# Kernel optimization log

Hardware: AMD Instinct MI355X
Metric: run time of the kernel (lower is better)

The kernel has to match this reference:

```python
import jax, jax.numpy as jnp
import numpy as np
import math

S, B, D, H = 2048, 2, 1024, 16
DK = D // H


def setup_inputs() -> dict:
    key = jax.random.key(0)
    ks = jax.random.split(key, 13)
    scale = 1.0 / math.sqrt(D)
    inp = {
        "query": jax.random.normal(ks[0], (S, B, D), jnp.float32),
        "key": jax.random.normal(ks[1], (S, B, D), jnp.float32),
        "value": jax.random.normal(ks[2], (S, B, D), jnp.float32),
        "mask": jax.random.normal(ks[3], (B, S, S), jnp.float32),
        # four Linear(d_model, d_model) layers: q, k, v, out. torch convention W:(out,in)
        "Wq": jax.random.normal(ks[4], (D, D), jnp.float32) * scale,
        "bq": jax.random.normal(ks[5], (D,), jnp.float32) * scale,
        "Wk": jax.random.normal(ks[6], (D, D), jnp.float32) * scale,
        "bk": jax.random.normal(ks[7], (D,), jnp.float32) * scale,
        "Wv": jax.random.normal(ks[8], (D, D), jnp.float32) * scale,
        "bv": jax.random.normal(ks[9], (D,), jnp.float32) * scale,
        "Wo": jax.random.normal(ks[10], (D, D), jnp.float32) * scale,
        "bo": jax.random.normal(ks[11], (D,), jnp.float32) * scale,
    }
    return inp


def reference(query, key, value, mask, Wq, bq, Wk, bk, Wv, bv, Wo, bo):
    # inputs are (tokens S, batch B, d_model D)
    def proj(x, W, b):  # torch Linear: x @ W.T + b, then split heads -> (B,H,S,DK)
        y = jnp.einsum('sbd,ed->sbe', x, W) + b
        return y.reshape(S, B, H, DK).transpose(1, 2, 0, 3)

    q = proj(query, Wq, bq)
    k = proj(key, Wk, bk)
    v = proj(value, Wv, bv)

    scores = jnp.einsum('bhsd,bhtd->bhst', q, k) / math.sqrt(DK)
    scores = scores + mask[:, None, :, :]  # broadcast over heads
    p_attn = jax.nn.softmax(scores, axis=-1)  # (B,H,S,S)

    x = jnp.einsum('bhst,bhtd->bhsd', p_attn, v)  # (B,H,S,DK)
    x = x.transpose(2, 0, 1, 3).reshape(S, B, D)  # (S,B,D)
    out = jnp.einsum('sbd,ed->sbe', x, Wo) + bo

    attn = p_attn.mean(axis=1)  # mean over heads -> (B,S,S)
    return out, attn
```

## Files before the change

kernel.cpp:

```cpp
#include <hip/hip_runtime.h>
#include <hip/hip_bf16.h>


#define S_LEN 2048
#define BATCH 2
#define DMODEL 1024
#define NH 16
#define DKH 64
#define SCALE 0.125f
#define QSCALE 0.180336878f
#define FMAX 20.0f
#define KSTRIDE 72

typedef __bf16 bf16_t;
typedef __attribute__((ext_vector_type(8))) __bf16 bf16x8;
typedef __attribute__((ext_vector_type(8))) unsigned short u16x8;
typedef __attribute__((ext_vector_type(4))) float f32x4;

__device__ __forceinline__ unsigned short f32_bf16_rne(float f) {
  union { float f; unsigned int u; } v; v.f = f;
  unsigned int u = v.u;
  u += 0x7fffu + ((u >> 16) & 1u);
  return (unsigned short)(u >> 16);
}
__device__ __forceinline__ float bf16u_f32(unsigned short us) {
  union { unsigned int u; float f; } v; v.u = ((unsigned int)us) << 16;
  return v.f;
}
__device__ __forceinline__ f32x4 mfma_bf16(bf16x8 a, bf16x8 b, f32x4 c) {
  return __builtin_amdgcn_mfma_f32_16x16x32_bf16(a, b, c, 0, 0, 0);
}
__device__ __forceinline__ float exp2_fast(float x) {
#if __has_builtin(__builtin_amdgcn_exp2f)
  return __builtin_amdgcn_exp2f(x);
#else
  return __expf(x * 0.69314718f);
#endif
}
__device__ __forceinline__ void gload16(const bf16_t* g, unsigned short* l) {
  __builtin_amdgcn_global_load_lds(
      (const __attribute__((address_space(1))) void*)g,
      (__attribute__((address_space(3))) void*)l, 16, 0, 0);
}

__global__ __launch_bounds__(256) void cvt_w_kernel(
    const float* __restrict__ w0, const float* __restrict__ w1,
    const float* __restrict__ w2, const float* __restrict__ w3,
    bf16_t* __restrict__ o0, bf16_t* __restrict__ o1,
    bf16_t* __restrict__ o2, bf16_t* __restrict__ o3) {
  const float* src; bf16_t* dst;
  switch (blockIdx.y) {
    case 0: src = w0; dst = o0; break;
    case 1: src = w1; dst = o1; break;
    case 2: src = w2; dst = o2; break;
    default: src = w3; dst = o3; break;
  }
  int i = (blockIdx.x * 256 + threadIdx.x) * 4;
  float4 v = *(const float4*)(src + i);
  union { unsigned short u[4]; uint2 q; } r;
  r.u[0] = f32_bf16_rne(v.x); r.u[1] = f32_bf16_rne(v.y);
  r.u[2] = f32_bf16_rne(v.z); r.u[3] = f32_bf16_rne(v.w);
  *(uint2*)(dst + i) = r.q;
}

__global__ __launch_bounds__(256) void cvt_x_kernel(
    const float* __restrict__ x0, const float* __restrict__ x1,
    const float* __restrict__ x2,
    bf16_t* __restrict__ o0, bf16_t* __restrict__ o1, bf16_t* __restrict__ o2) {
  const float* src; bf16_t* dst;
  switch (blockIdx.y) {
    case 0: src = x0; dst = o0; break;
    case 1: src = x1; dst = o1; break;
    default: src = x2; dst = o2; break;
  }
  int i = (blockIdx.x * 256 + threadIdx.x) * 4;
  float4 v = *(const float4*)(src + i);
  union { unsigned short u[4]; uint2 q; } r;
  r.u[0] = f32_bf16_rne(v.x); r.u[1] = f32_bf16_rne(v.y);
  r.u[2] = f32_bf16_rne(v.z); r.u[3] = f32_bf16_rne(v.w);
  *(uint2*)(dst + i) = r.q;
}

__global__ __launch_bounds__(256) void cvt_mask_kernel(
    const float* __restrict__ m, bf16_t* __restrict__ o) {
  int i = (blockIdx.x * 256 + threadIdx.x) * 4;
  float4 v = *(const float4*)(m + i);
  union { unsigned short u[4]; uint2 q; } r;
  r.u[0] = f32_bf16_rne(__expf(v.x - FMAX));
  r.u[1] = f32_bf16_rne(__expf(v.y - FMAX));
  r.u[2] = f32_bf16_rne(__expf(v.z - FMAX));
  r.u[3] = f32_bf16_rne(__expf(v.w - FMAX));
  *(uint2*)(o + i) = r.q;
}

__global__ __launch_bounds__(256) void proj_kernel(
    const bf16_t* __restrict__ Xq, const bf16_t* __restrict__ Xk, const bf16_t* __restrict__ Xv,
    const bf16_t* __restrict__ Wqb, const bf16_t* __restrict__ Wkb, const bf16_t* __restrict__ Wvb,
    const float* __restrict__ bq, const float* __restrict__ bk, const float* __restrict__ bv,
    bf16_t* __restrict__ qo, bf16_t* __restrict__ ko, bf16_t* __restrict__ vTo) {
  int mode = blockIdx.z;
  const bf16_t* X = (mode == 0) ? Xq : (mode == 1) ? Xk : Xv;
  const bf16_t* W = (mode == 0) ? Wqb : (mode == 1) ? Wkb : Wvb;
  const float* bias = (mode == 0) ? bq : (mode == 1) ? bk : bv;

  __shared__ __align__(16) unsigned short Alds[128 * 32];
  __shared__ __align__(16) unsigned short Blds[128 * 32];

  int tid = threadIdx.x;
  int wv = tid >> 6, lane = tid & 63, quad = lane >> 4, col = lane & 15;
  int wr = wv >> 1, wc = wv & 1;
  int rowbase = blockIdx.x * 128;
  int colbase = blockIdx.y * 128;

  int srow = tid >> 2;
  int sk8 = (tid & 3) * 8;
  const bf16_t* ga0 = X + (size_t)(rowbase + srow) * DMODEL + sk8;
  const bf16_t* gb0 = W + (size_t)(colbase + srow) * DMODEL + sk8;
  unsigned short* la0 = Alds + tid * 8;
  unsigned short* lb0 = Blds + tid * 8;

  f32x4 acc[4][4] = {};

  for (int k0 = 0; k0 < DMODEL; k0 += 32) {
    gload16(ga0 + k0, la0);
    gload16(ga0 + 64 * DMODEL + k0, la0 + 2048);
    gload16(gb0 + k0, lb0);
    gload16(gb0 + 64 * DMODEL + k0, lb0 + 2048);
    __syncthreads();

    union { u16x8 u; bf16x8 v; } af[4], bfr[4];
#pragma unroll
    for (int mi = 0; mi < 4; ++mi)
      af[mi].u = *(const u16x8*)(Alds + (wr * 64 + mi * 16 + col) * 32 + quad * 8);
#pragma unroll
    for (int ni = 0; ni < 4; ++ni)
      bfr[ni].u = *(const u16x8*)(Blds + (wc * 64 + ni * 16 + col) * 32 + quad * 8);
#pragma unroll
    for (int mi = 0; mi < 4; ++mi)
#pragma unroll
      for (int ni = 0; ni < 4; ++ni)
        acc[mi][ni] = mfma_bf16(af[mi].v, bfr[ni].v, acc[mi][ni]);
    __syncthreads();
  }

  float biasv[4];
#pragma unroll
  for (int ni = 0; ni < 4; ++ni)
    biasv[ni] = bias[colbase + wc * 64 + ni * 16 + col];

#pragma unroll
  for (int mi = 0; mi < 4; ++mi)
#pragma unroll
    for (int ni = 0; ni < 4; ++ni)
#pragma unroll
      for (int r = 0; r < 4; ++r) {
        int grow = rowbase + wr * 64 + mi * 16 + quad * 4 + r;
        int gcol = colbase + wc * 64 + ni * 16 + col;
        float val = acc[mi][ni][r] + biasv[ni];
        if (mode == 0) val *= QSCALE;
        unsigned short us = f32_bf16_rne(val);
        int s = grow >> 1, bb = grow & 1;
        int h = gcol >> 6, dk = gcol & 63;
        if (mode == 2) {
          ((unsigned short*)vTo)[((size_t)(bb * NH + h) * DKH + dk) * S_LEN + s] = us;
        } else {
          unsigned short* dst = (unsigned short*)(mode == 0 ? qo : ko);
          dst[((size_t)(bb * NH + h) * S_LEN + s) * DKH + dk] = us;
        }
      }
}

__global__ __launch_bounds__(512) void flash_kernel(
    const bf16_t* __restrict__ emb,
    const bf16_t* __restrict__ q_ws, const bf16_t* __restrict__ k_ws,
    const bf16_t* __restrict__ vT_ws,
    bf16_t* __restrict__ x_ws, float* __restrict__ rl_ws) {
  int tid = threadIdx.x;
  int w = tid >> 6, lane = tid & 63, quad = lane >> 4, col = lane & 15;
  int b = blockIdx.y, h = blockIdx.z;
  int s0 = blockIdx.x * 128 + w * 16;
  int bh = b * NH + h;

  __shared__ __align__(16) unsigned short Klds[64 * KSTRIDE];
  __shared__ __align__(16) unsigned short Vlds[64 * KSTRIDE];
  __shared__ __align__(16) unsigned short Plds[8][16 * KSTRIDE];
  unsigned short* pw = &Plds[w][0];

  const bf16_t* qh = q_ws + (size_t)bh * S_LEN * DKH;
  const bf16_t* kh = k_ws + (size_t)bh * S_LEN * DKH;
  const bf16_t* vh = vT_ws + (size_t)bh * DKH * S_LEN;
  const unsigned short* emrow = (const unsigned short*)emb +
      (size_t)b * S_LEN * S_LEN + (size_t)(s0 + quad * 4) * S_LEN;

  bf16x8 qf0 = *(const bf16x8*)(qh + (s0 + col) * DKH + quad * 8);
  bf16x8 qf1 = *(const bf16x8*)(qh + (s0 + col) * DKH + 32 + quad * 8);

  int srow = w * 8 + (lane >> 3), schunk = lane & 7;
  const unsigned short* kg = (const unsigned short*)(kh + (size_t)srow * DKH + schunk * 8);
  const unsigned short* vg = (const unsigned short*)(vh + (size_t)srow * S_LEN + schunk * 8);
  u16x8* kl = (u16x8*)(Klds + srow * KSTRIDE + schunk * 8);
  u16x8* vl = (u16x8*)(Vlds + srow * KSTRIDE + schunk * 8);

  int psw = (quad & 2) ? 16 : 0;
  int rsw = (col & 8) ? 16 : 0;

  f32x4 xacc[4] = {};
  f32x4 lacc = {};

  u16x8 kpre = *(const u16x8*)kg;
  u16x8 vpre = *(const u16x8*)vg;

  for (int t0 = 0; t0 < S_LEN; t0 += 64) {
    *kl = kpre;
    *vl = vpre;
    __syncthreads();

    if (t0 + 64 < S_LEN) {
      kpre = *(const u16x8*)(kg + (size_t)(t0 + 64) * DKH);
      vpre = *(const u16x8*)(vg + (t0 + 64));
    }

    float emv[4][4];
#pragma unroll
    for (int j = 0; j < 4; ++j)
#pragma unroll
      for (int r = 0; r < 4; ++r)
        emv[j][r] = bf16u_f32(emrow[r * S_LEN + t0 + j * 16 + col]);

    f32x4 C[4];
#pragma unroll
    for (int j = 0; j < 4; ++j) {
      int row = j * 16 + col;
      union { u16x8 u; bf16x8 v; } kb0, kb1;
      kb0.u = *(const u16x8*)(Klds + row * KSTRIDE + quad * 8);
      kb1.u = *(const u16x8*)(Klds + row * KSTRIDE + 32 + quad * 8);
      f32x4 z = {};
      C[j] = mfma_bf16(qf1, kb1.v, mfma_bf16(qf0, kb0.v, z));
    }

#pragma unroll
    for (int j = 0; j < 4; ++j) {
      float p0 = exp2_fast(C[j][0]) * emv[j][0];
      float p1 = exp2_fast(C[j][1]) * emv[j][1];
      float p2 = exp2_fast(C[j][2]) * emv[j][2];
      float p3 = exp2_fast(C[j][3]) * emv[j][3];
      lacc[0] += p0; lacc[1] += p1; lacc[2] += p2; lacc[3] += p3;
      unsigned int w01, w23;
      asm("v_cvt_pk_bf16_f32 %0, %1, %2" : "=v"(w01) : "v"(p0), "v"(p1));
      asm("v_cvt_pk_bf16_f32 %0, %1, %2" : "=v"(w23) : "v"(p2), "v"(p3));
      int tsw = (j * 16 + col) ^ psw;
      int rb = quad * 4;
      pw[(rb + 0) * KSTRIDE + tsw] = (unsigned short)(w01 & 0xffffu);
      pw[(rb + 1) * KSTRIDE + tsw] = (unsigned short)(w01 >> 16);
      pw[(rb + 2) * KSTRIDE + tsw] = (unsigned short)(w23 & 0xffffu);
      pw[(rb + 3) * KSTRIDE + tsw] = (unsigned short)(w23 >> 16);
    }

    union { u16x8 u; bf16x8 v; } pa0, pa1;
    pa0.u = *(const u16x8*)(pw + col * KSTRIDE + ((quad * 8) ^ rsw));
    pa1.u = *(const u16x8*)(pw + col * KSTRIDE + (32 + ((quad * 8) ^ rsw)));

#pragma unroll
    for (int ni = 0; ni < 4; ++ni) {
      int row = ni * 16 + col;
      union { u16x8 u; bf16x8 v; } vb0, vb1;
      vb0.u = *(const u16x8*)(Vlds + row * KSTRIDE + quad * 8);
      vb1.u = *(const u16x8*)(Vlds + row * KSTRIDE + 32 + quad * 8);
      xacc[ni] = mfma_bf16(pa1.v, vb1.v, mfma_bf16(pa0.v, vb0.v, xacc[ni]));
    }
    __syncthreads();
  }

  for (int d = 1; d < 16; d <<= 1)
    for (int r = 0; r < 4; ++r) lacc[r] += __shfl_xor(lacc[r], d, 64);
  float rl[4];
  for (int r = 0; r < 4; ++r) rl[r] = 1.0f / lacc[r];

  unsigned short* xo = (unsigned short*)x_ws;
  for (int ni = 0; ni < 4; ++ni)
    for (int r = 0; r < 4; ++r) {
      int sr = s0 + quad * 4 + r;
      xo[((size_t)bh * S_LEN + sr) * DKH + ni * 16 + col] =
          f32_bf16_rne(xacc[ni][r] * rl[r]);
    }
  if (col == 0)
    for (int r = 0; r < 4; ++r)
      rl_ws[bh * S_LEN + s0 + quad * 4 + r] = rl[r];
}

__global__ __launch_bounds__(256) void attn_kernel(
    const bf16_t* __restrict__ emb,
    const bf16_t* __restrict__ q_ws, const bf16_t* __restrict__ k_ws,
    const float* __restrict__ rl_ws,
    float* __restrict__ attn_out) {
  int tid = threadIdx.x;
  int w = tid >> 6, lane = tid & 63, quad = lane >> 4, col = lane & 15;
  int b = blockIdx.y;
  int s0 = blockIdx.x * 64 + w * 16;
  int t_base = blockIdx.z * 128;

  __shared__ __align__(16) unsigned short Klds[128 * KSTRIDE];

  const unsigned short* emrow = (const unsigned short*)emb +
      (size_t)b * S_LEN * S_LEN + (size_t)(s0 + quad * 4) * S_LEN + t_base;
  float emf[8][4];
  for (int j = 0; j < 8; ++j)
    for (int r = 0; r < 4; ++r)
      emf[j][r] = bf16u_f32(emrow[r * S_LEN + j * 16 + col]);

  f32x4 acc[8] = {};

  int srow_a = w * 8 + (lane >> 3), schunk_a = (lane & 7) * 8;
  const bf16_t* kh0 = k_ws + (size_t)(b * NH) * S_LEN * DKH;

  u16x8 kpre[4];
#pragma unroll
  for (int i = 0; i < 4; ++i)
    kpre[i] = *(const u16x8*)(kh0 + (size_t)(t_base + i * 32 + srow_a) * DKH + schunk_a);

  for (int h = 0; h < NH; ++h) {
    int bh = b * NH + h;
    const bf16_t* qh = q_ws + (size_t)bh * S_LEN * DKH;

#pragma unroll
    for (int i = 0; i < 4; ++i)
      *(u16x8*)(Klds + (i * 32 + srow_a) * KSTRIDE + schunk_a) = kpre[i];
    __syncthreads();

    if (h + 1 < NH) {
      const bf16_t* khn = kh0 + (size_t)(h + 1) * S_LEN * DKH;
#pragma unroll
      for (int i = 0; i < 4; ++i)
        kpre[i] = *(const u16x8*)(khn + (size_t)(t_base + i * 32 + srow_a) * DKH + schunk_a);
    }

    bf16x8 qf0 = *(const bf16x8*)(qh + (s0 + col) * DKH + quad * 8);
    bf16x8 qf1 = *(const bf16x8*)(qh + (s0 + col) * DKH + 32 + quad * 8);
    float rl4[4];
    for (int r = 0; r < 4; ++r) rl4[r] = rl_ws[bh * S_LEN + s0 + quad * 4 + r];

#pragma unroll
    for (int j = 0; j < 8; ++j) {
      int row = j * 16 + col;
      union { u16x8 u; bf16x8 v; } kb0, kb1;
      kb0.u = *(const u16x8*)(Klds + row * KSTRIDE + quad * 8);
      kb1.u = *(const u16x8*)(Klds + row * KSTRIDE + 32 + quad * 8);
      f32x4 z = {};
      f32x4 C = mfma_bf16(qf1, kb1.v, mfma_bf16(qf0, kb0.v, z));
#pragma unroll
      for (int r = 0; r < 4; ++r) {
        float t = exp2_fast(C[r]) * emf[j][r];
        acc[j][r] = fmaf(t, rl4[r], acc[j][r]);
      }
    }
    __syncthreads();
  }

  for (int j = 0; j < 8; ++j)
    for (int r = 0; r < 4; ++r)
      attn_out[((size_t)b * S_LEN + s0 + quad * 4 + r) * S_LEN + t_base + j * 16 + col] =
          acc[j][r] * (1.0f / NH);
}

__global__ __launch_bounds__(256) void outproj_kernel(
    const bf16_t* __restrict__ x_ws, const bf16_t* __restrict__ Wob,
    const float* __restrict__ bo, float* __restrict__ out) {
  __shared__ __align__(16) unsigned short Alds[128 * 32];
  __shared__ __align__(16) unsigned short Blds[128 * 32];

  int tid = threadIdx.x;
  int wv = tid >> 6, lane = tid & 63, quad = lane >> 4, col = lane & 15;
  int wr = wv >> 1, wc = wv & 1;
  int rowbase = blockIdx.x * 128;
  int colbase = blockIdx.y * 128;

  int srow = tid >> 2;
  int sk8 = (tid & 3) * 8;
  int r0 = rowbase + srow;
  int s0a = r0 >> 1, b0a = r0 & 1;
  int r1 = r0 + 64;
  int s1a = r1 >> 1, b1a = r1 & 1;
  const bf16_t* gb0 = Wob + (size_t)(colbase + srow) * DMODEL + sk8;
  unsigned short* la0 = Alds + tid * 8;
  unsigned short* lb0 = Blds + tid * 8;

  f32x4 acc[4][4] = {};

  for (int k0 = 0; k0 < DMODEL; k0 += 32) {
    int h = k0 >> 6, dk = (k0 & 63) + sk8;
    gload16(x_ws + ((size_t)(b0a * NH + h) * S_LEN + s0a) * DKH + dk, la0);
    gload16(x_ws + ((size_t)(b1a * NH + h) * S_LEN + s1a) * DKH + dk, la0 + 2048);
    gload16(gb0 + k0, lb0);
    gload16(gb0 + 64 * DMODEL + k0, lb0 + 2048);
    __syncthreads();

    union { u16x8 u; bf16x8 v; } af[4], bfr[4];
#pragma unroll
    for (int mi = 0; mi < 4; ++mi)
      af[mi].u = *(const u16x8*)(Alds + (wr * 64 + mi * 16 + col) * 32 + quad * 8);
#pragma unroll
    for (int ni = 0; ni < 4; ++ni)
      bfr[ni].u = *(const u16x8*)(Blds + (wc * 64 + ni * 16 + col) * 32 + quad * 8);
#pragma unroll
    for (int mi = 0; mi < 4; ++mi)
#pragma unroll
      for (int ni = 0; ni < 4; ++ni)
        acc[mi][ni] = mfma_bf16(af[mi].v, bfr[ni].v, acc[mi][ni]);
    __syncthreads();
  }

  float biasv[4];
#pragma unroll
  for (int ni = 0; ni < 4; ++ni)
    biasv[ni] = bo[colbase + wc * 64 + ni * 16 + col];

#pragma unroll
  for (int mi = 0; mi < 4; ++mi)
#pragma unroll
    for (int ni = 0; ni < 4; ++ni)
#pragma unroll
      for (int r = 0; r < 4; ++r) {
        int grow = rowbase + wr * 64 + mi * 16 + quad * 4 + r;
        int gcol = colbase + wc * 64 + ni * 16 + col;
        out[(size_t)grow * DMODEL + gcol] = acc[mi][ni][r] + biasv[ni];
      }
}

extern "C" void kernel_launch(void* const* d_in, const int* in_sizes, int n_in,
                              void* d_out, int out_size, void* d_ws, size_t ws_size,
                              hipStream_t stream) {
  const float* query = (const float*)d_in[0];
  const float* key_  = (const float*)d_in[1];
  const float* value = (const float*)d_in[2];
  const float* mask  = (const float*)d_in[3];
  const float* Wq = (const float*)d_in[4];
  const float* bq = (const float*)d_in[5];
  const float* Wk = (const float*)d_in[6];
  const float* bk = (const float*)d_in[7];
  const float* Wv = (const float*)d_in[8];
  const float* bv = (const float*)d_in[9];
  const float* Wo = (const float*)d_in[10];
  const float* bo = (const float*)d_in[11];

  char* ws = (char*)d_ws;
  bf16_t* q_ws  = (bf16_t*)(ws + 0);
  bf16_t* k_ws  = (bf16_t*)(ws + 8388608);
  bf16_t* vT_ws = (bf16_t*)(ws + 16777216);
  bf16_t* x_ws  = (bf16_t*)(ws + 25165824);
  float*  rl_ws = (float*)(ws + 33554432);
  bf16_t* Wqb = (bf16_t*)(ws + 33816576);
  bf16_t* Wkb = (bf16_t*)(ws + 35913728);
  bf16_t* Wvb = (bf16_t*)(ws + 38010880);
  bf16_t* Wob = (bf16_t*)(ws + 40108032);
  bf16_t* Xq_b = x_ws;
  bf16_t* Xk_b = (bf16_t*)(ws + 42205184);
  bf16_t* Xv_b = (bf16_t*)(ws + 50593792);
  bf16_t* emb  = (bf16_t*)(ws + 42205184);

  float* outp  = (float*)d_out;
  float* attnp = outp + (size_t)S_LEN * BATCH * DMODEL;

  cvt_w_kernel<<<dim3(1024, 4), 256, 0, stream>>>(Wq, Wk, Wv, Wo, Wqb, Wkb, Wvb, Wob);
  cvt_x_kernel<<<dim3(4096, 3), 256, 0, stream>>>(query, key_, value, Xq_b, Xk_b, Xv_b);
  proj_kernel<<<dim3(32, 8, 3), 256, 0, stream>>>(Xq_b, Xk_b, Xv_b,
                                                  Wqb, Wkb, Wvb, bq, bk, bv,
                                                  q_ws, k_ws, vT_ws);
  cvt_mask_kernel<<<dim3(8192), 256, 0, stream>>>(mask, emb);
  flash_kernel<<<dim3(16, 2, 16), 512, 0, stream>>>(emb, q_ws, k_ws, vT_ws, x_ws, rl_ws);
  attn_kernel<<<dim3(32, 2, 16), 256, 0, stream>>>(emb, q_ws, k_ws, rl_ws, attnp);
  outproj_kernel<<<dim3(32, 8), 256, 0, stream>>>(x_ws, Wob, bo, outp);
}
```

Measured before the change: 350.3 us.

## Restructure flash kernel: transposed MFMA keeps P in registers, two query tiles per wave

The flash kernel now computes S^T = K·Q^T, so each lane holds probabilities along the key dimension. K rows are loaded into LDS in a permuted order so those probabilities can feed the P·V MFMA straight from registers, which removes the per-wave LDS round trip for P. Each wave now handles two 16-row query tiles, so every K/V fragment read from LDS is reused twice. Blocks shrink to 256 threads on a 1D grid whose index mapping spreads (batch, head) pairs across neighbouring blocks. The cost is more registers per wave and fewer waves per block.

```diff
diff --git a/kernel.cpp b/kernel.cpp
--- a/kernel.cpp
+++ b/kernel.cpp
@@ -15,6 +15,7 @@
 typedef __bf16 bf16_t;
 typedef __attribute__((ext_vector_type(8))) __bf16 bf16x8;
 typedef __attribute__((ext_vector_type(8))) unsigned short u16x8;
+typedef __attribute__((ext_vector_type(4))) unsigned short u16x4;
 typedef __attribute__((ext_vector_type(4))) float f32x4;
 
 __device__ __forceinline__ unsigned short f32_bf16_rne(float f) {
@@ -36,6 +37,11 @@
 #else
   return __expf(x * 0.69314718f);
 #endif
+}
+__device__ __forceinline__ unsigned int cvtpk(float lo, float hi) {
+  unsigned int r;
+  asm("v_cvt_pk_bf16_f32 %0, %1, %2" : "=v"(r) : "v"(lo), "v"(hi));
+  return r;
 }
 __device__ __forceinline__ void gload16(const bf16_t* g, unsigned short* l) {
   __builtin_amdgcn_global_load_lds(
@@ -170,122 +176,145 @@
       }
 }
 
-__global__ __launch_bounds__(512) void flash_kernel(
+__global__ __launch_bounds__(256) void flash_kernel(
     const bf16_t* __restrict__ emb,
     const bf16_t* __restrict__ q_ws, const bf16_t* __restrict__ k_ws,
     const bf16_t* __restrict__ vT_ws,
     bf16_t* __restrict__ x_ws, float* __restrict__ rl_ws) {
   int tid = threadIdx.x;
   int w = tid >> 6, lane = tid & 63, quad = lane >> 4, col = lane & 15;
-  int b = blockIdx.y, h = blockIdx.z;
-  int s0 = blockIdx.x * 128 + w * 16;
-  int bh = b * NH + h;
+
+  int bid = blockIdx.x;
+  int wi = bid >> 3;
+  int bh = (bid & 7) * 4 + (wi & 3);
+  int qblk = wi >> 2;
+  int b = bh >> 4;
+  int s0 = qblk * 128 + w * 32;
+  int sA = s0, sB = s0 + 16;
 
   __shared__ __align__(16) unsigned short Klds[64 * KSTRIDE];
   __shared__ __align__(16) unsigned short Vlds[64 * KSTRIDE];
-  __shared__ __align__(16) unsigned short Plds[8][16 * KSTRIDE];
-  unsigned short* pw = &Plds[w][0];
 
   const bf16_t* qh = q_ws + (size_t)bh * S_LEN * DKH;
   const bf16_t* kh = k_ws + (size_t)bh * S_LEN * DKH;
   const bf16_t* vh = vT_ws + (size_t)bh * DKH * S_LEN;
-  const unsigned short* emrow = (const unsigned short*)emb +
-      (size_t)b * S_LEN * S_LEN + (size_t)(s0 + quad * 4) * S_LEN;
-
-  bf16x8 qf0 = *(const bf16x8*)(qh + (s0 + col) * DKH + quad * 8);
-  bf16x8 qf1 = *(const bf16x8*)(qh + (s0 + col) * DKH + 32 + quad * 8);
-
-  int srow = w * 8 + (lane >> 3), schunk = lane & 7;
-  const unsigned short* kg = (const unsigned short*)(kh + (size_t)srow * DKH + schunk * 8);
-  const unsigned short* vg = (const unsigned short*)(vh + (size_t)srow * S_LEN + schunk * 8);
-  u16x8* kl = (u16x8*)(Klds + srow * KSTRIDE + schunk * 8);
-  u16x8* vl = (u16x8*)(Vlds + srow * KSTRIDE + schunk * 8);
-
-  int psw = (quad & 2) ? 16 : 0;
-  int rsw = (col & 8) ? 16 : 0;
-
-  f32x4 xacc[4] = {};
-  f32x4 lacc = {};
-
-  u16x8 kpre = *(const u16x8*)kg;
-  u16x8 vpre = *(const u16x8*)vg;
+  const unsigned short* emA = (const unsigned short*)emb +
+      (size_t)b * S_LEN * S_LEN + (size_t)(sA + col) * S_LEN;
+  const unsigned short* emB = emA + (size_t)16 * S_LEN;
+
+  bf16x8 qA0 = *(const bf16x8*)(qh + (sA + col) * DKH + quad * 8);
+  bf16x8 qA1 = *(const bf16x8*)(qh + (sA + col) * DKH + 32 + quad * 8);
+  bf16x8 qB0 = *(const bf16x8*)(qh + (sB + col) * DKH + quad * 8);
+  bf16x8 qB1 = *(const bf16x8*)(qh + (sB + col) * DKH + 32 + quad * 8);
+
+  int row1 = tid >> 3, row2 = row1 + 32;
+  int ch = (tid & 7) * 8;
+  int pi1 = (row1 & 32) + ((row1 & 16) >> 2) + ((row1 & 12) << 1) + (row1 & 3);
+  int pi2 = (row2 & 32) + ((row2 & 16) >> 2) + ((row2 & 12) << 1) + (row2 & 3);
+  const unsigned short* kg1 = (const unsigned short*)kh + (size_t)pi1 * DKH + ch;
+  const unsigned short* kg2 = (const unsigned short*)kh + (size_t)pi2 * DKH + ch;
+  const unsigned short* vg1 = (const unsigned short*)vh + (size_t)row1 * S_LEN + ch;
+  const unsigned short* vg2 = (const unsigned short*)vh + (size_t)row2 * S_LEN + ch;
+  u16x8* kl1 = (u16x8*)(Klds + row1 * KSTRIDE + ch);
+  u16x8* kl2 = (u16x8*)(Klds + row2 * KSTRIDE + ch);
+  u16x8* vl1 = (u16x8*)(Vlds + row1 * KSTRIDE + ch);
+  u16x8* vl2 = (u16x8*)(Vlds + row2 * KSTRIDE + ch);
+
+  f32x4 xA[4] = {}, xB[4] = {};
+  float lsumA = 0.0f, lsumB = 0.0f;
+
+  u16x8 kp1 = *(const u16x8*)kg1;
+  u16x8 kp2 = *(const u16x8*)kg2;
+  u16x8 vp1 = *(const u16x8*)vg1;
+  u16x8 vp2 = *(const u16x8*)vg2;
 
   for (int t0 = 0; t0 < S_LEN; t0 += 64) {
-    *kl = kpre;
-    *vl = vpre;
+    *kl1 = kp1; *kl2 = kp2; *vl1 = vp1; *vl2 = vp2;
     __syncthreads();
 
     if (t0 + 64 < S_LEN) {
-      kpre = *(const u16x8*)(kg + (size_t)(t0 + 64) * DKH);
-      vpre = *(const u16x8*)(vg + (t0 + 64));
-    }
-
-    float emv[4][4];
-#pragma unroll
-    for (int j = 0; j < 4; ++j)
-#pragma unroll
-      for (int r = 0; r < 4; ++r)
-        emv[j][r] = bf16u_f32(emrow[r * S_LEN + t0 + j * 16 + col]);
-
-    f32x4 C[4];
+      kp1 = *(const u16x8*)(kg1 + (size_t)(t0 + 64) * DKH);
+      kp2 = *(const u16x8*)(kg2 + (size_t)(t0 + 64) * DKH);
+      vp1 = *(const u16x8*)(vg1 + (t0 + 64));
+      vp2 = *(const u16x8*)(vg2 + (t0 + 64));
+    }
+
+    u16x4 emA4[4], emB4[4];
 #pragma unroll
     for (int j = 0; j < 4; ++j) {
+      int f = t0 + ((j >> 1) << 5) + ((j & 1) << 2) + quad * 8;
+      emA4[j] = *(const u16x4*)(emA + f);
+      emB4[j] = *(const u16x4*)(emB + f);
+    }
+
+    f32x4 CA[4], CB[4];
+#pragma unroll
+    for (int j = 0; j < 4; ++j) {
+      union { u16x8 u; bf16x8 v; } kb0, kb1;
       int row = j * 16 + col;
-      union { u16x8 u; bf16x8 v; } kb0, kb1;
       kb0.u = *(const u16x8*)(Klds + row * KSTRIDE + quad * 8);
       kb1.u = *(const u16x8*)(Klds + row * KSTRIDE + 32 + quad * 8);
       f32x4 z = {};
-      C[j] = mfma_bf16(qf1, kb1.v, mfma_bf16(qf0, kb0.v, z));
-    }
-
+      CA[j] = mfma_bf16(kb1.v, qA1, mfma_bf16(kb0.v, qA0, z));
+      CB[j] = mfma_bf16(kb1.v, qB1, mfma_bf16(kb0.v, qB0, z));
+    }
+
+    unsigned int PA[8], PB[8];
 #pragma unroll
     for (int j = 0; j < 4; ++j) {
-      float p0 = exp2_fast(C[j][0]) * emv[j][0];
-      float p1 = exp2_fast(C[j][1]) * emv[j][1];
-      float p2 = exp2_fast(C[j][2]) * emv[j][2];
-      float p3 = exp2_fast(C[j][3]) * emv[j][3];
-      lacc[0] += p0; lacc[1] += p1; lacc[2] += p2; lacc[3] += p3;
-      unsigned int w01, w23;
-      asm("v_cvt_pk_bf16_f32 %0, %1, %2" : "=v"(w01) : "v"(p0), "v"(p1));
-      asm("v_cvt_pk_bf16_f32 %0, %1, %2" : "=v"(w23) : "v"(p2), "v"(p3));
-      int tsw = (j * 16 + col) ^ psw;
-      int rb = quad * 4;
-      pw[(rb + 0) * KSTRIDE + tsw] = (unsigned short)(w01 & 0xffffu);
-      pw[(rb + 1) * KSTRIDE + tsw] = (unsigned short)(w01 >> 16);
-      pw[(rb + 2) * KSTRIDE + tsw] = (unsigned short)(w23 & 0xffffu);
-      pw[(rb + 3) * KSTRIDE + tsw] = (unsigned short)(w23 >> 16);
-    }
-
-    union { u16x8 u; bf16x8 v; } pa0, pa1;
-    pa0.u = *(const u16x8*)(pw + col * KSTRIDE + ((quad * 8) ^ rsw));
-    pa1.u = *(const u16x8*)(pw + col * KSTRIDE + (32 + ((quad * 8) ^ rsw)));
+      float a0 = exp2_fast(CA[j][0]) * bf16u_f32(emA4[j][0]);
+      float a1 = exp2_fast(CA[j][1]) * bf16u_f32(emA4[j][1]);
+      float a2 = exp2_fast(CA[j][2]) * bf16u_f32(emA4[j][2]);
+      float a3 = exp2_fast(CA[j][3]) * bf16u_f32(emA4[j][3]);
+      lsumA += (a0 + a1) + (a2 + a3);
+      PA[j * 2] = cvtpk(a0, a1);
+      PA[j * 2 + 1] = cvtpk(a2, a3);
+      float b0 = exp2_fast(CB[j][0]) * bf16u_f32(emB4[j][0]);
+      float b1 = exp2_fast(CB[j][1]) * bf16u_f32(emB4[j][1]);
+      float b2 = exp2_fast(CB[j][2]) * bf16u_f32(emB4[j][2]);
+      float b3 = exp2_fast(CB[j][3]) * bf16u_f32(emB4[j][3]);
+      lsumB += (b0 + b1) + (b2 + b3);
+      PB[j * 2] = cvtpk(b0, b1);
+      PB[j * 2 + 1] = cvtpk(b2, b3);
+    }
+    union { unsigned int u32[4]; bf16x8 v; } bA0, bA1, bB0, bB1;
+#pragma unroll
+    for (int i = 0; i < 4; ++i) {
+      bA0.u32[i] = PA[i]; bA1.u32[i] = PA[4 + i];
+      bB0.u32[i] = PB[i]; bB1.u32[i] = PB[4 + i];
+    }
 
 #pragma unroll
     for (int ni = 0; ni < 4; ++ni) {
+      union { u16x8 u; bf16x8 v; } vb0, vb1;
       int row = ni * 16 + col;
-      union { u16x8 u; bf16x8 v; } vb0, vb1;
       vb0.u = *(const u16x8*)(Vlds + row * KSTRIDE + quad * 8);
       vb1.u = *(const u16x8*)(Vlds + row * KSTRIDE + 32 + quad * 8);
-      xacc[ni] = mfma_bf16(pa1.v, vb1.v, mfma_bf16(pa0.v, vb0.v, xacc[ni]));
-    }
-    __syncthreads();
-  }
-
-  for (int d = 1; d < 16; d <<= 1)
-    for (int r = 0; r < 4; ++r) lacc[r] += __shfl_xor(lacc[r], d, 64);
-  float rl[4];
-  for (int r = 0; r < 4; ++r) rl[r] = 1.0f / lacc[r];
+      xA[ni] = mfma_bf16(vb1.v, bA1.v, mfma_bf16(vb0.v, bA0.v, xA[ni]));
+      xB[ni] = mfma_bf16(vb1.v, bB1.v, mfma_bf16(vb0.v, bB0.v, xB[ni]));
+    }
+    __syncthreads();
+  }
+
+  lsumA += __shfl_xor(lsumA, 16, 64); lsumA += __shfl_xor(lsumA, 32, 64);
+  lsumB += __shfl_xor(lsumB, 16, 64); lsumB += __shfl_xor(lsumB, 32, 64);
+  float rlA = 1.0f / lsumA, rlB = 1.0f / lsumB;
 
   unsigned short* xo = (unsigned short*)x_ws;
-  for (int ni = 0; ni < 4; ++ni)
-    for (int r = 0; r < 4; ++r) {
-      int sr = s0 + quad * 4 + r;
-      xo[((size_t)bh * S_LEN + sr) * DKH + ni * 16 + col] =
-          f32_bf16_rne(xacc[ni][r] * rl[r]);
-    }
-  if (col == 0)
-    for (int r = 0; r < 4; ++r)
-      rl_ws[bh * S_LEN + s0 + quad * 4 + r] = rl[r];
+#pragma unroll
+  for (int ni = 0; ni < 4; ++ni) {
+    uint2 wa, wb;
+    wa.x = cvtpk(xA[ni][0] * rlA, xA[ni][1] * rlA);
+    wa.y = cvtpk(xA[ni][2] * rlA, xA[ni][3] * rlA);
+    wb.x = cvtpk(xB[ni][0] * rlB, xB[ni][1] * rlB);
+    wb.y = cvtpk(xB[ni][2] * rlB, xB[ni][3] * rlB);
+    *(uint2*)(xo + ((size_t)bh * S_LEN + sA + col) * DKH + ni * 16 + quad * 4) = wa;
+    *(uint2*)(xo + ((size_t)bh * S_LEN + sB + col) * DKH + ni * 16 + quad * 4) = wb;
+  }
+  if (quad == 0) {
+    rl_ws[(size_t)bh * S_LEN + sA + col] = rlA;
+    rl_ws[(size_t)bh * S_LEN + sB + col] = rlB;
+  }
 }
 
 __global__ __launch_bounds__(256) void attn_kernel(
@@ -466,7 +495,7 @@
                                                   Wqb, Wkb, Wvb, bq, bk, bv,
                                                   q_ws, k_ws, vT_ws);
   cvt_mask_kernel<<<dim3(8192), 256, 0, stream>>>(mask, emb);
-  flash_kernel<<<dim3(16, 2, 16), 512, 0, stream>>>(emb, q_ws, k_ws, vT_ws, x_ws, rl_ws);
+  flash_kernel<<<dim3(512), 256, 0, stream>>>(emb, q_ws, k_ws, vT_ws, x_ws, rl_ws);
   attn_kernel<<<dim3(32, 2, 16), 256, 0, stream>>>(emb, q_ws, k_ws, rl_ws, attnp);
   outproj_kernel<<<dim3(32, 8), 256, 0, stream>>>(x_ws, Wob, bo, outp);
 }
```

After: 338.9 us. 1.03x faster.
